# Optimization experiments

Measured on AMD Instinct MI355X. Metric: run time of the kernel, lower is better.

Reference implementation:

```python
import jax, jax.numpy as jnp
import numpy as np

RADIUS = 3
NPATCH = 9          # patch_sampling_num
DROP_RATE = 0.1
TEMP = 0.5
BW = 1.0            # band_width
K, STRIDE, PAD = 7, 2, 3          # conv params (kernel_size, stride, padding)
POOL_K, POOL_S, POOL_P = 3, 2, 1  # maxpool params
OUTDIM = 64


def _compute_mask(x_old, out_shape):
    """Replicates Info_Dropout's no_grad mask construction."""
    B, C, H, W = x_old.shape
    pl = PAD + RADIUS
    pr = PAD + RADIUS + 1
    padded = jnp.pad(x_old, ((0, 0), (0, 0), (pl, pr), (pl, pr)))
    hd = H + 2 * PAD  # spatial extent of the sliced region (torch: [radius:-radius-1])

    # torch.randint offsets in [-radius, radius]; concrete ints (fixed seed)
    rng = np.random.default_rng(0)
    si = rng.integers(-RADIUS, RADIUS + 1, NPATCH)
    sj = rng.integers(-RADIUS, RADIUS + 1, NPATCH)

    base = padded[:, :, RADIUS:RADIUS + hd, RADIUS:RADIUS + hd]
    dists = []
    for i, j in zip(si, sj):  # fixed small loop over 9 sampled patch offsets
        shifted = padded[:, :, RADIUS + i:RADIUS + i + hd, RADIUS + j:RADIUS + j + hd]
        dists.append(((base - shifted) ** 2).sum(axis=1))  # sum over indim channels
    distance = jnp.stack(dists, axis=1)  # (B, 9, hd, hd)

    # all-ones depthwise KxK stride-S conv == per-channel box sum
    distance = jax.lax.reduce_window(
        distance, 0.0, jax.lax.add,
        (1, 1, K, K), (1, 1, STRIDE, STRIDE), 'VALID')
    distance = jnp.exp(-distance / distance.mean() / 2.0 / (BW ** 2))

    # all-ones 1x1 conv 9->outdim == sum over 9 channels, replicated
    prob = (distance.sum(axis=1, keepdims=True) / NPATCH) ** (1.0 / TEMP)  # (B,1,h,w)
    prob = jnp.broadcast_to(prob, (B, OUTDIM) + prob.shape[2:])

    # prob = -maxpool(-prob) == min-pool; torch maxpool pads with -inf
    prob = -jax.lax.reduce_window(
        -prob, -jnp.inf, jax.lax.max,
        (1, 1, POOL_K, POOL_K), (1, 1, POOL_S, POOL_S),
        [(0, 0), (0, 0), (POOL_P, POOL_P), (POOL_P, POOL_P)])
    prob = prob / prob.sum(axis=(-2, -1), keepdims=True)

    Bo, Co, h, w = out_shape
    nsamp = int(DROP_RATE * h * w)
    flat = prob.reshape(Bo * Co, h * w)
    logits = jnp.log(flat + 1e-8)  # multinomial(prob + 1e-8) with replacement
    key = jax.random.key(42)
    choice = jax.random.categorical(key, logits, axis=-1, shape=(nsamp, Bo * Co)).T  # (BC, nsamp)
    mask = jnp.ones((Bo * Co, h * w), flat.dtype)
    mask = mask.at[jnp.arange(Bo * Co)[:, None], choice].set(0.0)
    return mask.reshape(out_shape)


def setup_inputs() -> dict:
    key = jax.random.key(0)
    k1, k2 = jax.random.split(key)
    x_old = jax.random.normal(k1, (32, 3, 224, 224), dtype=jnp.float32)
    x = jax.random.normal(k2, (32, 64, 56, 56), dtype=jnp.float32)
    return {"x_old": x_old, "x": x}


def reference(x_old, x):
    mask = _compute_mask(x_old, x.shape)
    return x * mask
```

## Files before the change

kernel.cpp:

```cpp
#include <hip/hip_runtime.h>
#include <math.h>
#include <stdint.h>

#pragma clang fp contract(off)

#define NDIST   3612672
#define NPMAP   401408
#define NPOOL   100352
#define NSAMP_T 641024
#define NTASK2  1282048
#define NMEANB  882

__device__ __align__(16) float g_dist[NDIST];
__device__ __align__(16) float g_pmap[NPMAP];
__device__ __align__(16) float g_pooled[NPOOL];
__device__ __align__(16) float g_logits[NPOOL];
__device__ __align__(16) float g_pM[NTASK2];
__device__ __align__(16) int   g_pJ[NTASK2];
__device__ float g_partial[NMEANB];
__device__ float g_lmax[32];
__device__ float g_mean[1];
__device__ int   g_sij[18];

__device__ __forceinline__ uint32_t ss_hash(uint32_t value, uint32_t& hc) {
  value ^= hc; hc *= 0x931e8875u; value *= hc; value ^= value >> 16; return value;
}
__device__ __forceinline__ uint32_t ss_mix(uint32_t x, uint32_t y) {
  uint32_t r = x * 0xca01f9ddu - y * 0x4973f715u;
  r ^= r >> 16; return r;
}

__global__ void k_rng() {
  if (threadIdx.x != 0 || blockIdx.x != 0) return;
  uint32_t pool[4];
  uint32_t hc = 0x43b0d7e5u;
  for (int i = 0; i < 4; ++i) pool[i] = ss_hash(0u, hc);
  for (int is = 0; is < 4; ++is)
    for (int id = 0; id < 4; ++id)
      if (is != id) pool[id] = ss_mix(pool[id], ss_hash(pool[is], hc));
  uint32_t hb = 0x8b51f9ddu;
  uint32_t w[8];
  for (int i = 0; i < 8; ++i) {
    uint32_t dv = pool[i & 3];
    dv ^= hb; hb *= 0x58f38dedu; dv *= hb; dv ^= dv >> 16; w[i] = dv;
  }
  uint64_t gs[4];
  for (int i = 0; i < 4; ++i) gs[i] = (uint64_t)w[2*i] | ((uint64_t)w[2*i+1] << 32);
  const __uint128_t MUL = (((__uint128_t)0x2360ED051FC65DA4ull) << 64) | 0x4385DF649FCCF645ull;
  __uint128_t initstate = (((__uint128_t)gs[0]) << 64) | gs[1];
  __uint128_t initseq   = (((__uint128_t)gs[2]) << 64) | gs[3];
  __uint128_t inc   = (initseq << 1) | 1;
  __uint128_t state = 0;
  state = state * MUL + inc;
  state += initstate;
  state = state * MUL + inc;

  bool has32 = false; uint32_t saved32 = 0;
  auto next32 = [&]() -> uint32_t {
    if (has32) { has32 = false; return saved32; }
    state = state * MUL + inc;
    uint64_t xo = (uint64_t)(state >> 64) ^ (uint64_t)state;
    uint32_t rot = (uint32_t)(state >> 122) & 63u;
    uint64_t v = (xo >> rot) | (xo << ((64u - rot) & 63u));
    has32 = true; saved32 = (uint32_t)(v >> 32);
    return (uint32_t)v;
  };

  for (int k = 0; k < 18; ++k) {
    uint64_t m = (uint64_t)next32() * 7ull;
    uint32_t leftover = (uint32_t)m;
    if (leftover < 7u) {
      while (leftover < 4u) { m = (uint64_t)next32() * 7ull; leftover = (uint32_t)m; }
    }
    g_sij[k] = (int)(uint32_t)(m >> 32) - 3;
  }
}

__global__ __launch_bounds__(256) void k_dist(const float* __restrict__ xold) {
  int idx = blockIdx.x * 256 + threadIdx.x;
  if (idx >= NDIST) return;
  int ox = idx % 112; int tt = idx / 112;
  int oy = tt % 112;  tt /= 112;
  int p = tt % 9;     int b = tt / 9;
  int si = g_sij[p], sj = g_sij[9 + p];
  const float* xb = xold + (size_t)b * 3 * 224 * 224;
  float acc = 0.f;
  for (int kh = 0; kh < 7; ++kh) {
    int hb = 2 * oy + kh - 3;
    int hs = hb + si;
    for (int kw = 0; kw < 7; ++kw) {
      int wb = 2 * ox + kw - 3;
      int wsf = wb + sj;
      float s = 0.f;
      for (int c = 0; c < 3; ++c) {
        const float* xc = xb + c * 224 * 224;
        float bv = (hb >= 0 && hb < 224 && wb >= 0 && wb < 224) ? xc[hb * 224 + wb] : 0.f;
        float sv = (hs >= 0 && hs < 224 && wsf >= 0 && wsf < 224) ? xc[hs * 224 + wsf] : 0.f;
        float d = bv - sv;
        s = s + d * d;
      }
      acc = acc + s;
    }
  }
  g_dist[idx] = acc;
}

__global__ __launch_bounds__(256) void k_mean1() {
  __shared__ float red[256];
  int base = blockIdx.x * 4096;
  float acc = 0.f;
  #pragma unroll
  for (int i = 0; i < 4; ++i) {
    float4 v = *(const float4*)(g_dist + base + threadIdx.x * 4 + i * 1024);
    acc = acc + v.x + v.y + v.z + v.w;
  }
  red[threadIdx.x] = acc;
  __syncthreads();
  for (int s = 128; s > 0; s >>= 1) {
    if (threadIdx.x < s) red[threadIdx.x] += red[threadIdx.x + s];
    __syncthreads();
  }
  if (threadIdx.x == 0) g_partial[blockIdx.x] = red[0];
}
__global__ void k_mean2() {
  if (threadIdx.x != 0 || blockIdx.x != 0) return;
  float acc = 0.f;
  for (int i = 0; i < NMEANB; ++i) acc = acc + g_partial[i];
  g_mean[0] = acc / 3612672.0f;
}

__global__ __launch_bounds__(256) void k_prob1() {
  int idx = blockIdx.x * 256 + threadIdx.x;
  if (idx >= NPMAP) return;
  int xy = idx % 12544; int b = idx / 12544;
  float m = g_mean[0];
  float ssum = 0.f;
  for (int p = 0; p < 9; ++p) {
    float d = g_dist[(size_t)(b * 9 + p) * 12544 + xy];
    float t = (-d / m) / 2.0f;
    float e = expf(t);
    ssum = ssum + e;
  }
  float q = ssum / 9.0f;
  g_pmap[idx] = q * q;
}

__global__ __launch_bounds__(256) void k_pool() {
  int idx = blockIdx.x * 256 + threadIdx.x;
  if (idx >= NPOOL) return;
  int ox = idx % 56; int tt = idx / 56;
  int oy = tt % 56;  int b = tt / 56;
  float mn = INFINITY;
  for (int kh = 0; kh < 3; ++kh) {
    int y = 2 * oy - 1 + kh; if (y < 0 || y >= 112) continue;
    for (int kw = 0; kw < 3; ++kw) {
      int x = 2 * ox - 1 + kw; if (x < 0 || x >= 112) continue;
      mn = fminf(mn, g_pmap[(size_t)(b * 112 + y) * 112 + x]);
    }
  }
  g_pooled[idx] = mn;
}

__global__ void k_norm() {
  int b = threadIdx.x;
  if (b >= 32 || blockIdx.x != 0) return;
  const float* P = g_pooled + b * 3136;
  float s = 0.f;
  for (int i = 0; i < 3136; ++i) s = s + P[i];
  float lm = -INFINITY;
  for (int i = 0; i < 3136; ++i) {
    float fl = P[i] / s;
    float lg = logf(fl + 1e-8f);
    g_logits[b * 3136 + i] = lg;
    lm = fmaxf(lm, lg);
  }
  g_lmax[b] = lm;
}

__global__ __launch_bounds__(256) void k_copy(const float4* __restrict__ x, float4* __restrict__ out) {
  int i = blockIdx.x * 256 + threadIdx.x;
  out[i] = x[i];
}

__device__ __forceinline__ uint32_t rotl32(uint32_t x, int r) { return __builtin_rotateleft32(x, r); }
__device__ __forceinline__ void threefry2x32(uint32_t x0, uint32_t x1, uint32_t& o0, uint32_t& o1) {
  const uint32_t ks0 = 0u, ks1 = 42u, ks2 = 0x1BD11BDAu ^ 0u ^ 42u;
  x0 += ks0; x1 += ks1;
#define TFR(r) { x0 += x1; x1 = rotl32(x1, (r)); x1 ^= x0; }
  TFR(13) TFR(15) TFR(26) TFR(6)  x0 += ks1; x1 += ks2 + 1u;
  TFR(17) TFR(29) TFR(16) TFR(24) x0 += ks2; x1 += ks0 + 2u;
  TFR(13) TFR(15) TFR(26) TFR(6)  x0 += ks0; x1 += ks1 + 3u;
  TFR(17) TFR(29) TFR(16) TFR(24) x0 += ks1; x1 += ks2 + 4u;
  TFR(13) TFR(15) TFR(26) TFR(6)  x0 += ks2; x1 += ks0 + 5u;
#undef TFR
  o0 = x0; o1 = x1;
}

__device__ __forceinline__ uint32_t random_bits_at(uint32_t idx) {
  uint32_t o0, o1; threefry2x32(0u, idx, o0, o1);
  return o0 ^ o1;
}

#define TF_R(S) \
  "v_add_u32 %0, %0, %1\n\t" \
  "v_add_u32 %2, %2, %3\n\t" \
  "v_alignbit_b32 %1, %1, %1, " S "\n\t" \
  "v_alignbit_b32 %3, %3, %3, " S "\n\t" \
  "v_xor_b32 %1, %1, %0\n\t" \
  "v_xor_b32 %3, %3, %2\n\t"
#define TF_GX TF_R("19") TF_R("17") TF_R("6") TF_R("26")
#define TF_GY TF_R("15") TF_R("3") TF_R("16") TF_R("8")

__device__ __forceinline__ void tf2_dual(uint32_t inA, uint32_t inB,
                                         uint32_t& outA, uint32_t& outB) {
  uint32_t a0 = 0u, a1 = inA + 42u;
  uint32_t b0 = 0u, b1 = inB + 42u;
  asm(TF_GX
      "v_add_u32 %0, 42, %0\n\t"
      "v_add_u32 %2, 42, %2\n\t"
      "v_add_u32 %1, 0x1bd11bf1, %1\n\t"
      "v_add_u32 %3, 0x1bd11bf1, %3\n\t"
      TF_GY
      "v_add_u32 %0, 0x1bd11bf0, %0\n\t"
      "v_add_u32 %2, 0x1bd11bf0, %2\n\t"
      "v_add_u32 %1, 2, %1\n\t"
      "v_add_u32 %3, 2, %3\n\t"
      TF_GX
      "v_add_u32 %1, 45, %1\n\t"
      "v_add_u32 %3, 45, %3\n\t"
      TF_GY
      "v_add_u32 %0, 42, %0\n\t"
      "v_add_u32 %2, 42, %2\n\t"
      "v_add_u32 %1, 0x1bd11bf4, %1\n\t"
      "v_add_u32 %3, 0x1bd11bf4, %3\n\t"
      TF_GX
      "v_add_u32 %0, 0x1bd11bf0, %0\n\t"
      "v_add_u32 %2, 0x1bd11bf0, %2\n\t"
      "v_add_u32 %1, 5, %1\n\t"
      "v_add_u32 %3, 5, %3\n\t"
      "v_xor_b32 %0, %0, %1\n\t"
      "v_xor_b32 %2, %2, %3"
      : "+v"(a0), "+v"(a1), "+v"(b0), "+v"(b1));
  outA = a0; outB = b0;
}

__device__ __forceinline__ float gumbel_ocml(uint32_t mant) {
  float uni;
  if (mant == 0u) uni = 1.17549435e-38f;
  else uni = __uint_as_float(0x3f800000u | mant) - 1.0f;
  float l1 = logf(uni);
  float n1 = -l1;
  float l2 = logf(n1);
  return -l2;
}


#define TOP2_UPD(x, jj) { \
  bool g = (x) > w1; \
  j1 = g ? (jj) : j1; \
  w2 = max(min((x), w1), w2); \
  w1 = max(w1, (x)); }

__global__ __launch_bounds__(512) void k_samp() {
  int lane  = threadIdx.x & 63;
  int wtask = blockIdx.x * 8 + (threadIdx.x >> 6);
  int t = wtask >> 1;
  int h = wtask & 1;
  int b = (t & 2047) >> 6;
  const float* Lh = g_logits + b * 3136 + h * 1568;
  float Lmx = g_lmax[b];
  uint32_t vbase = (uint32_t)t * 3136u + (uint32_t)(h * 1568);

  uint32_t w1, w2 = 0u; int j1;
  uint32_t vidx = vbase + (uint32_t)lane;
  {
    uint32_t xA, xB;
    tf2_dual(vidx, vidx + 64u, xA, xB);
    w1 = xA; j1 = lane;
    TOP2_UPD(xB, lane + 64)
    vidx += 128u;
  }
  for (int k = 1; k < 12; ++k) {
    uint32_t xA, xB;
    tf2_dual(vidx, vidx + 64u, xA, xB);
    int jA = lane + (k << 7);
    TOP2_UPD(xA, jA)
    TOP2_UPD(xB, jA + 64)
    vidx += 128u;
  }
  if (lane < 32) {
    uint32_t x = random_bits_at(vbase + 1536u + (uint32_t)lane);
    TOP2_UPD(x, 1536 + lane)
  }

  float val1 = Lh[j1] + gumbel_ocml(w1 >> 9);
  float T0 = val1;
  #pragma unroll
  for (int off = 32; off; off >>= 1) T0 = fmaxf(T0, __shfl_xor(T0, off));

  float Tp = T0 - Lmx - 1e-3f;
  uint32_t mthr = 0u;
  if (Tp > -80.0f) {
    float u_thr = expf(-expf(-Tp));
    int mi = (int)(u_thr * 8388608.0f) - 8;
    mthr = mi > 0 ? (uint32_t)mi : 0u;
  }
  uint32_t B0 = mthr << 9;

  float bestV; int bestJ;
  if (w1 >= B0) { bestV = val1; bestJ = j1; }
  else          { bestV = -INFINITY; bestJ = 0x7fffffff; }

  bool flag = (w2 >= B0) || (B0 == 0u);
  if (__any(flag)) {
    if (flag) {
      uint32_t vi = vbase + (uint32_t)lane;
      for (int k = 0; k < 25; ++k) {
        if (k == 24 && lane >= 32) break;
        uint32_t x = random_bits_at(vi);
        if (x >= B0) {
          int jj = lane + (k << 6);
          float v = Lh[jj] + gumbel_ocml(x >> 9);
          if (v > bestV || (v == bestV && jj < bestJ)) { bestV = v; bestJ = jj; }
        }
        vi += 64u;
      }
    }
  }

  #pragma unroll
  for (int off = 32; off; off >>= 1) {
    float ov = __shfl_xor(bestV, off);
    int   oj = __shfl_xor(bestJ, off);
    if (ov > bestV || (ov == bestV && oj < bestJ)) { bestV = ov; bestJ = oj; }
  }
  if (lane == 0) {
    g_pM[wtask] = bestV;
    g_pJ[wtask] = h * 1568 + bestJ;
  }
}

__global__ __launch_bounds__(256) void k_merge(float* __restrict__ out) {
  int t = blockIdx.x * 256 + threadIdx.x;
  float M0 = g_pM[2 * t], M1 = g_pM[2 * t + 1];
  int j = (M1 > M0) ? g_pJ[2 * t + 1] : g_pJ[2 * t];
  int r = t & 2047;
  out[(size_t)r * 3136 + (size_t)j] = 0.0f;
}

extern "C" void kernel_launch(void* const* d_in, const int* in_sizes, int n_in,
                              void* d_out, int out_size, void* d_ws, size_t ws_size,
                              hipStream_t stream) {
  (void)in_sizes; (void)n_in; (void)d_ws; (void)ws_size; (void)out_size;
  const float* x_old = (const float*)d_in[0];
  const float* x     = (const float*)d_in[1];
  float* out = (float*)d_out;

  k_rng  <<<1,     64, 0, stream>>>();
  k_dist <<<14112, 256, 0, stream>>>(x_old);
  k_mean1<<<NMEANB,256, 0, stream>>>();
  k_mean2<<<1,     64, 0, stream>>>();
  k_prob1<<<1568,  256, 0, stream>>>();
  k_pool <<<392,   256, 0, stream>>>();
  k_norm <<<1,     64, 0, stream>>>();
  k_copy <<<6272,  256, 0, stream>>>((const float4*)x, (float4*)out);
  k_samp <<<160256, 512, 0, stream>>>();
  k_merge<<<2504,  256, 0, stream>>>(out);
}
```

Baseline: 4.960 ms.

## Cache random bits in registers and prefilter Gumbel candidates; parallelize logit normalization

The sampler now keeps all 25 per-lane random words in registers from the first pass, so they are not regenerated with threefry in the second pass. A cheap log2-based lower bound on each Gumbel value skips the exact double-log for candidates that cannot beat the wave threshold. The top-2 tracking is dropped in favor of a per-slot wave-uniform check. The serial normalization kernel is split into a row-sum kernel and a 32-block parallel log/max kernel. This raises register pressure, and the approximate bound must never reject a true winner for results to stay exact.

```diff
diff --git a/kernel.cpp b/kernel.cpp
--- a/kernel.cpp
+++ b/kernel.cpp
@@ -18,6 +18,7 @@
 __device__ __align__(16) float g_pM[NTASK2];
 __device__ __align__(16) int   g_pJ[NTASK2];
 __device__ float g_partial[NMEANB];
+__device__ float g_rowsum[32];
 __device__ float g_lmax[32];
 __device__ float g_mean[1];
 __device__ int   g_sij[18];
@@ -161,20 +162,34 @@
   g_pooled[idx] = mn;
 }
 
-__global__ void k_norm() {
+__global__ void k_norm1() {
   int b = threadIdx.x;
   if (b >= 32 || blockIdx.x != 0) return;
   const float* P = g_pooled + b * 3136;
   float s = 0.f;
   for (int i = 0; i < 3136; ++i) s = s + P[i];
+  g_rowsum[b] = s;
+}
+
+__global__ __launch_bounds__(256) void k_norm2() {
+  __shared__ float red[4];
+  int b = blockIdx.x;
+  float s = g_rowsum[b];
+  const float* P = g_pooled + b * 3136;
   float lm = -INFINITY;
-  for (int i = 0; i < 3136; ++i) {
+  for (int i = threadIdx.x; i < 3136; i += 256) {
     float fl = P[i] / s;
     float lg = logf(fl + 1e-8f);
     g_logits[b * 3136 + i] = lg;
     lm = fmaxf(lm, lg);
   }
-  g_lmax[b] = lm;
+  #pragma unroll
+  for (int off = 32; off; off >>= 1) lm = fmaxf(lm, __shfl_xor(lm, off));
+  int wid = threadIdx.x >> 6;
+  if ((threadIdx.x & 63) == 0) red[wid] = lm;
+  __syncthreads();
+  if (threadIdx.x == 0)
+    g_lmax[b] = fmaxf(fmaxf(red[0], red[1]), fmaxf(red[2], red[3]));
 }
 
 __global__ __launch_bounds__(256) void k_copy(const float4* __restrict__ x, float4* __restrict__ out) {
@@ -255,12 +270,6 @@
 }
 
 
-#define TOP2_UPD(x, jj) { \
-  bool g = (x) > w1; \
-  j1 = g ? (jj) : j1; \
-  w2 = max(min((x), w1), w2); \
-  w1 = max(w1, (x)); }
-
 __global__ __launch_bounds__(512) void k_samp() {
   int lane  = threadIdx.x & 63;
   int wtask = blockIdx.x * 8 + (threadIdx.x >> 6);
@@ -271,26 +280,26 @@
   float Lmx = g_lmax[b];
   uint32_t vbase = (uint32_t)t * 3136u + (uint32_t)(h * 1568);
 
-  uint32_t w1, w2 = 0u; int j1;
+  uint32_t bb[25];
+  uint32_t w1; int j1;
   uint32_t vidx = vbase + (uint32_t)lane;
+  tf2_dual(vidx, vidx + 64u, bb[0], bb[1]);
+  w1 = bb[0]; j1 = lane;
+  { bool g = bb[1] > w1; j1 = g ? (lane + 64) : j1; w1 = g ? bb[1] : w1; }
+  vidx += 128u;
+  #pragma unroll
+  for (int k = 1; k < 12; ++k) {
+    tf2_dual(vidx, vidx + 64u, bb[2*k], bb[2*k+1]);
+    int jA = lane + (k << 7);
+    { bool g = bb[2*k]   > w1; j1 = g ? jA        : j1; w1 = g ? bb[2*k]   : w1; }
+    { bool g = bb[2*k+1] > w1; j1 = g ? (jA + 64) : j1; w1 = g ? bb[2*k+1] : w1; }
+    vidx += 128u;
+  }
   {
-    uint32_t xA, xB;
-    tf2_dual(vidx, vidx + 64u, xA, xB);
-    w1 = xA; j1 = lane;
-    TOP2_UPD(xB, lane + 64)
-    vidx += 128u;
-  }
-  for (int k = 1; k < 12; ++k) {
-    uint32_t xA, xB;
-    tf2_dual(vidx, vidx + 64u, xA, xB);
-    int jA = lane + (k << 7);
-    TOP2_UPD(xA, jA)
-    TOP2_UPD(xB, jA + 64)
-    vidx += 128u;
-  }
-  if (lane < 32) {
     uint32_t x = random_bits_at(vbase + 1536u + (uint32_t)lane);
-    TOP2_UPD(x, 1536 + lane)
+    x = (lane < 32) ? x : 0u;
+    bb[24] = x;
+    bool g = x > w1; j1 = g ? (1536 + lane) : j1; w1 = g ? x : w1;
   }
 
   float val1 = Lh[j1] + gumbel_ocml(w1 >> 9);
@@ -307,23 +316,23 @@
   }
   uint32_t B0 = mthr << 9;
 
-  float bestV; int bestJ;
-  if (w1 >= B0) { bestV = val1; bestJ = j1; }
-  else          { bestV = -INFINITY; bestJ = 0x7fffffff; }
-
-  bool flag = (w2 >= B0) || (B0 == 0u);
-  if (__any(flag)) {
-    if (flag) {
-      uint32_t vi = vbase + (uint32_t)lane;
-      for (int k = 0; k < 25; ++k) {
-        if (k == 24 && lane >= 32) break;
-        uint32_t x = random_bits_at(vi);
-        if (x >= B0) {
-          int jj = lane + (k << 6);
-          float v = Lh[jj] + gumbel_ocml(x >> 9);
+  float bestV = -INFINITY; int bestJ = 0x7fffffff;
+  #pragma unroll
+  for (int k = 0; k < 25; ++k) {
+    uint32_t x = bb[k];
+    bool pass = (x >= B0);
+    if (k == 24) pass = pass && (lane < 32);
+    if (__any(pass)) {
+      if (pass) {
+        int jj = lane + (k << 6);
+        uint32_t mant = x >> 9;
+        float zf = (float)(0x800000u - mant);
+        float gub = fmaf(__log2f(zf), -0.6931472f, 15.943385f);
+        float Lj = Lh[jj];
+        if (Lj + gub > T0) {
+          float v = Lj + gumbel_ocml(mant);
           if (v > bestV || (v == bestV && jj < bestJ)) { bestV = v; bestJ = jj; }
         }
-        vi += 64u;
       }
     }
   }
@@ -362,7 +371,8 @@
   k_mean2<<<1,     64, 0, stream>>>();
   k_prob1<<<1568,  256, 0, stream>>>();
   k_pool <<<392,   256, 0, stream>>>();
-  k_norm <<<1,     64, 0, stream>>>();
+  k_norm1<<<1,     64, 0, stream>>>();
+  k_norm2<<<32,   256, 0, stream>>>();
   k_copy <<<6272,  256, 0, stream>>>((const float4*)x, (float4*)out);
   k_samp <<<160256, 512, 0, stream>>>();
   k_merge<<<2504,  256, 0, stream>>>(out);
```

Result: faster. 4.683 ms (-5.6%).
